# Kernel optimization log

Measured on AMD Instinct MI355X. Metric: run time of the kernel, lower is better.

Reference implementation:

```python
import jax, jax.numpy as jnp
import numpy as np

B, S, D, H = 2, 2048, 2048, 16
HD = D // H


def setup_inputs() -> dict:
    key = jax.random.key(0)
    kx, = jax.random.split(key, 1)
    return {
        "x": jax.random.normal(kx, (B, S, D), dtype=jnp.float32),
        "q_mask": jnp.ones((D, D), dtype=jnp.float32),
        "k_mask": jnp.ones((D, D), dtype=jnp.float32),
        "v_mask": jnp.ones((D, D), dtype=jnp.float32),
        "out_mask": jnp.ones((D, D), dtype=jnp.float32),
        "head_mask": jnp.ones((H,), dtype=jnp.float32),
        "attention_mask": jnp.ones((B, S), dtype=jnp.float32),
        "shared_weight": jnp.float32(1.0),
    }


def reference(x, q_mask, k_mask, v_mask, out_mask, head_mask, attention_mask, shared_weight):
    b, s, d = x.shape
    scale = jnp.float32(HD) ** -0.5

    def shared_linear(inp, mask):
        # F.linear(x, mask * shared_weight): out = inp @ (mask*sw).T
        return jnp.einsum("bsd,ed->bse", inp, mask * shared_weight)

    q = shared_linear(x, q_mask).reshape(b, s, H, HD).transpose(0, 2, 1, 3)  # [B,H,S,HD]
    k = shared_linear(x, k_mask).reshape(b, s, H, HD).transpose(0, 2, 1, 3)
    v = shared_linear(x, v_mask).reshape(b, s, H, HD).transpose(0, 2, 1, 3)

    hm = head_mask.reshape(1, H, 1, 1)
    q, k, v = q * hm, k * hm, v * hm

    scores = jnp.einsum("bhqd,bhkd->bhqk", q, k) * scale  # [B,H,S,S]

    # causal mask: upper triangle (j > i) -> -inf
    causal = jnp.triu(jnp.ones((s, s), dtype=bool), k=1)
    scores = jnp.where(causal, -jnp.inf, scores)

    # additive attention mask: (1 - m) * -10000, broadcast [B,1,1,S]
    scores = scores + (1.0 - attention_mask)[:, None, None, :] * -10000.0

    attn = jax.nn.softmax(scores, axis=-1)  # dropout is identity in eval / p=0

    out = jnp.einsum("bhqk,bhkd->bhqd", attn, v)          # [B,H,S,HD]
    out = out.transpose(0, 2, 1, 3).reshape(b, s, d)       # [B,S,D]
    return shared_linear(out, out_mask)
```

## Files before the change

kernel.cpp:

```cpp
#include <hip/hip_runtime.h>

#define B_  2
#define S_  2048
#define D_  2048
#define H_  16
#define HD_ 128

typedef __bf16 bf16;
typedef __bf16 bf16x4 __attribute__((ext_vector_type(4)));
typedef __bf16 bf16x8 __attribute__((ext_vector_type(8)));
typedef float  f32x4  __attribute__((ext_vector_type(4)));

__device__ __forceinline__ void gld_lds16(const void* g, void* l) {
    __builtin_amdgcn_global_load_lds(
        (const __attribute__((address_space(1))) unsigned int*)g,
        (__attribute__((address_space(3))) unsigned int*)l, 16, 0, 0);
}

__global__ __launch_bounds__(256)
void precast_kernel(const float* __restrict__ x, bf16* __restrict__ xh,
                    bf16* __restrict__ xl) {
    int i = (blockIdx.x * 256 + threadIdx.x) * 8;
    float4 a = *(const float4*)(x + i);
    float4 b = *(const float4*)(x + i + 4);
    float av[8] = {a.x, a.y, a.z, a.w, b.x, b.y, b.z, b.w};
    bf16x8 h8, l8;
#pragma unroll
    for (int e = 0; e < 8; e++) {
        bf16 hv = (bf16)av[e];
        h8[e] = hv;
        l8[e] = (bf16)(av[e] - (float)hv);
    }
    *(bf16x8*)(xh + i) = h8;
    *(bf16x8*)(xl + i) = l8;
}

__global__ __launch_bounds__(256)
void transpose_v(const bf16* __restrict__ vp, bf16* __restrict__ vt) {
    const int bh = blockIdx.x >> 5;
    const int s0 = (blockIdx.x & 31) * 64;
    const int t = threadIdx.x;
    __shared__ bf16 tile[128 * 72];
    const bf16* src = vp + (size_t)bh * S_ * HD_;
    bf16* dst = vt + (size_t)bh * HD_ * S_;
    {
        int r = t >> 2;
        int g = (t & 3) * 4;
#pragma unroll
        for (int w = 0; w < 4; w++) {
            bf16x8 v8 = *(const bf16x8*)&src[(size_t)(s0 + r) * HD_ + (g + w) * 8];
#pragma unroll
            for (int e = 0; e < 8; e++) tile[((g + w) * 8 + e) * 72 + r] = v8[e];
        }
    }
    __syncthreads();
    {
        int d = t >> 1;
        int sg0 = (t & 1) * 4;
#pragma unroll
        for (int w = 0; w < 4; w++) {
            int sg = sg0 + w;
            *(bf16x8*)&dst[(size_t)d * S_ + s0 + sg * 8] =
                *(const bf16x8*)&tile[d * 72 + sg * 8];
        }
    }
}

#define BK 64

template<int MODE>
__global__ __launch_bounds__(256, 3)
void gemm_nt(const bf16* __restrict__ Ah_g, const bf16* __restrict__ Al_g,
             const float* __restrict__ B0, const float* __restrict__ B1,
             const float* __restrict__ B2,
             const float* __restrict__ swp, const float* __restrict__ hm,
             bf16* __restrict__ qh_, bf16* __restrict__ ql_,
             bf16* __restrict__ kh_, bf16* __restrict__ kl_,
             bf16* __restrict__ vp_, float* __restrict__ Cf) {
    const int K = D_;
    __shared__ bf16 Ah[128 * 64];
    __shared__ bf16 Al[128 * 64];
    __shared__ bf16 Bs[128 * 64];
    const int t = threadIdx.x;
    const int wave = t >> 6, lane = t & 63;
    const int wr = wave >> 1, wc = wave & 1;
    const int m0 = blockIdx.y * 128, n0 = blockIdx.x * 128;
    const int lrow = lane & 15, lquad = lane >> 4;
    const float sw = swp[0];

    const int which = (MODE == 0) ? (n0 >> 11) : 0;
    const bool split = (MODE == 0) && (which < 2);

    const float* Bp;
    if (MODE == 0) {
        Bp = (which == 0) ? B0 : ((which == 1) ? B1 : B2);
        Bp += (size_t)(n0 & (D_ - 1)) * K;
    } else {
        Bp = B0 + (size_t)n0 * K;
    }

    const int srow8 = lane >> 3;
    const int sgrp  = lane & 7;
    const int g0 = (lquad)     ^ (lrow & 7);
    const int g1 = (lquad + 4) ^ (lrow & 7);

    f32x4 acc[4][4];
#pragma unroll
    for (int i = 0; i < 4; i++)
#pragma unroll
        for (int j = 0; j < 4; j++) acc[i][j] = (f32x4){0.f, 0.f, 0.f, 0.f};

    for (int k0 = 0; k0 < K; k0 += BK) {
#pragma unroll
        for (int p = 0; p < 4; p++) {
            int r = wave * 32 + p * 8 + srow8;
            int gcol = (sgrp ^ (r & 7)) * 8;
            gld_lds16(Ah_g + (size_t)(m0 + r) * K + k0 + gcol,
                      &Ah[(wave * 32 + p * 8) * 64]);
            if (split)
                gld_lds16(Al_g + (size_t)(m0 + r) * K + k0 + gcol,
                          &Al[(wave * 32 + p * 8) * 64]);
        }
#pragma unroll
        for (int p = 0; p < 4; p++) {
            int r = p * 32 + (t >> 3);
            int gcol = (sgrp ^ (r & 7)) * 8;
            const float* bp = Bp + (size_t)r * K + k0 + gcol;
            float4 blo = *(const float4*)bp;
            float4 bhi = *(const float4*)(bp + 4);
            bf16x8 b8;
            b8[0] = (bf16)(blo.x * sw); b8[1] = (bf16)(blo.y * sw);
            b8[2] = (bf16)(blo.z * sw); b8[3] = (bf16)(blo.w * sw);
            b8[4] = (bf16)(bhi.x * sw); b8[5] = (bf16)(bhi.y * sw);
            b8[6] = (bf16)(bhi.z * sw); b8[7] = (bf16)(bhi.w * sw);
            *(bf16x8*)&Bs[r * 64 + sgrp * 8] = b8;
        }
        __syncthreads();

#pragma unroll
        for (int kk = 0; kk < 2; kk++) {
            const int gA = kk ? g1 : g0;
            bf16x8 afh[4], afl[4], bfr[4];
#pragma unroll
            for (int i = 0; i < 4; i++) {
                int row = wr * 64 + i * 16 + lrow;
                afh[i] = *(const bf16x8*)&Ah[row * 64 + gA * 8];
                if (split) afl[i] = *(const bf16x8*)&Al[row * 64 + gA * 8];
            }
#pragma unroll
            for (int j = 0; j < 4; j++) {
                int row = wc * 64 + j * 16 + lrow;
                bfr[j] = *(const bf16x8*)&Bs[row * 64 + gA * 8];
            }
#pragma unroll
            for (int i = 0; i < 4; i++)
#pragma unroll
                for (int j = 0; j < 4; j++) {
                    acc[i][j] = __builtin_amdgcn_mfma_f32_16x16x32_bf16(
                        afh[i], bfr[j], acc[i][j], 0, 0, 0);
                    if (split)
                        acc[i][j] = __builtin_amdgcn_mfma_f32_16x16x32_bf16(
                            afl[i], bfr[j], acc[i][j], 0, 0, 0);
                }
        }
        __syncthreads();
    }

#pragma unroll
    for (int i = 0; i < 4; i++) {
#pragma unroll
        for (int j = 0; j < 4; j++) {
#pragma unroll
            for (int r = 0; r < 4; r++) {
                int m = m0 + wr * 64 + i * 16 + lquad * 4 + r;
                int n = n0 + wc * 64 + j * 16 + lrow;
                float v = acc[i][j][r];
                if (MODE == 0) {
                    int e = n & (D_ - 1);
                    int h = e >> 7, hd = e & (HD_ - 1);
                    int b = m >> 11, s = m & (S_ - 1);
                    v *= hm[h];
                    size_t idx = (((size_t)b * H_ + h) * S_ + s) * HD_ + hd;
                    if (which == 2) {
                        vp_[idx] = (bf16)v;
                    } else {
                        bf16 hv = (bf16)v;
                        bf16 lv = (bf16)(v - (float)hv);
                        if (which == 0) { qh_[idx] = hv; ql_[idx] = lv; }
                        else            { kh_[idx] = hv; kl_[idx] = lv; }
                    }
                } else {
                    Cf[(size_t)m * D_ + n] = v;
                }
            }
        }
    }
}

__global__ __launch_bounds__(256, 3)
void attn_kernel(const bf16* __restrict__ qh_, const bf16* __restrict__ ql_,
                 const bf16* __restrict__ kh_, const bf16* __restrict__ kl_,
                 const bf16* __restrict__ vt_, const float* __restrict__ am,
                 bf16* __restrict__ outp) {
    const int bh = blockIdx.x & 31;
    const int qblk = 31 - (blockIdx.x >> 5);
    const int b = bh >> 4, h = bh & 15;
    const int i0 = qblk * 64;
    const int t = threadIdx.x, wave = t >> 6, lane = t & 63;
    const int lrow = lane & 15, quad = lane >> 4;

    __shared__ bf16 sh[26624];
    bf16* skh = sh;
    bf16* skl = sh + 8192;
    bf16* svt = sh + 16384;
    bf16* sp  = sh + 24576 + wave * 512;

    const size_t kbase = (size_t)bh * S_ * HD_;
    const size_t vbase = (size_t)bh * HD_ * S_;

    const int qrow = i0 + wave * 16 + lrow;
    bf16x8 qhf[4], qlf[4];
#pragma unroll
    for (int c = 0; c < 4; c++) {
        qhf[c] = *(const bf16x8*)&qh_[kbase + (size_t)qrow * HD_ + c * 32 + quad * 8];
        qlf[c] = *(const bf16x8*)&ql_[kbase + (size_t)qrow * HD_ + c * 32 + quad * 8];
    }

    bf16x8 ones8;
#pragma unroll
    for (int e = 0; e < 8; e++) ones8[e] = (bf16)1.0f;

    float m_i[4];
    f32x4 O[8], Ol;
#pragma unroll
    for (int r = 0; r < 4; r++) m_i[r] = -INFINITY;
#pragma unroll
    for (int n2 = 0; n2 < 8; n2++) O[n2] = (f32x4){0.f, 0.f, 0.f, 0.f};
    Ol = (f32x4){0.f, 0.f, 0.f, 0.f};

    const float scale = 0.08838834764831845f;
    const int iwmin = i0 + wave * 16;
    const int iwmax = iwmin + 15;
    const int nch = (i0 + 64) >> 5;

    {
#pragma unroll
        for (int p = 0; p < 2; p++) {
            int rb = wave * 8 + p * 4;
            int r  = rb + (lane >> 4);
            int gl = ((lane & 15) ^ (r & 7)) * 8;
            gld_lds16(kh_ + kbase + (size_t)r * HD_ + gl, skh + rb * 128);
            gld_lds16(kl_ + kbase + (size_t)r * HD_ + gl, skl + rb * 128);
        }
#pragma unroll
        for (int p = 0; p < 2; p++) {
            int db = wave * 32 + p * 16;
            int d  = db + (lane >> 2);
            int gl = ((lane & 3) ^ (d & 3)) * 8;
            gld_lds16(vt_ + vbase + (size_t)d * S_ + gl, svt + db * 32);
        }
    }

    for (int c = 0; c < nch; c++) {
        __syncthreads();
        if (c + 1 < nch) {
            const int j0s = (c + 1) * 32;
            bf16* dkh = skh + ((c + 1) & 1) * 4096;
            bf16* dkl = skl + ((c + 1) & 1) * 4096;
            bf16* dvt = svt + ((c + 1) & 1) * 4096;
#pragma unroll
            for (int p = 0; p < 2; p++) {
                int rb = wave * 8 + p * 4;
                int r  = rb + (lane >> 4);
                int gl = ((lane & 15) ^ (r & 7)) * 8;
                gld_lds16(kh_ + kbase + (size_t)(j0s + r) * HD_ + gl, dkh + rb * 128);
                gld_lds16(kl_ + kbase + (size_t)(j0s + r) * HD_ + gl, dkl + rb * 128);
            }
#pragma unroll
            for (int p = 0; p < 2; p++) {
                int db = wave * 32 + p * 16;
                int d  = db + (lane >> 2);
                int gl = ((lane & 3) ^ (d & 3)) * 8;
                gld_lds16(vt_ + vbase + (size_t)d * S_ + j0s + gl, dvt + db * 32);
            }
        }

        const int j0 = c * 32;
        if (j0 > iwmax) continue;

        const bf16* kH = skh + (c & 1) * 4096;
        const bf16* kL = skl + (c & 1) * 4096;
        const bf16* vT = svt + (c & 1) * 4096;

        float amadd0 = (1.0f - am[b * S_ + j0 + lrow])      * -10000.0f;
        float amadd1 = (1.0f - am[b * S_ + j0 + 16 + lrow]) * -10000.0f;

        f32x4 s4[2];
        s4[0] = (f32x4){0.f, 0.f, 0.f, 0.f};
        s4[1] = (f32x4){0.f, 0.f, 0.f, 0.f};
#pragma unroll
        for (int cg = 0; cg < 4; cg++) {
#pragma unroll
            for (int nt = 0; nt < 2; nt++) {
                int ka = (nt * 16 + lrow) * 128 + (((cg * 4 + quad) ^ (lrow & 7)) * 8);
                bf16x8 kb8 = *(const bf16x8*)&kH[ka];
                bf16x8 lb8 = *(const bf16x8*)&kL[ka];
                s4[nt] = __builtin_amdgcn_mfma_f32_16x16x32_bf16(qhf[cg], kb8, s4[nt], 0, 0, 0);
                s4[nt] = __builtin_amdgcn_mfma_f32_16x16x32_bf16(qhf[cg], lb8, s4[nt], 0, 0, 0);
                s4[nt] = __builtin_amdgcn_mfma_f32_16x16x32_bf16(qlf[cg], kb8, s4[nt], 0, 0, 0);
            }
        }

        const bool msk = (j0 + 31 > iwmin);
#pragma unroll
        for (int r = 0; r < 4; r++) {
            const int irow = iwmin + quad * 4 + r;
            float x0 = s4[0][r] * scale + amadd0;
            float x1 = s4[1][r] * scale + amadd1;
            if (msk) {
                if (j0 + lrow > irow)      x0 = -INFINITY;
                if (j0 + 16 + lrow > irow) x1 = -INFINITY;
            }
            float mx = fmaxf(x0, x1);
#pragma unroll
            for (int off = 1; off < 16; off <<= 1) mx = fmaxf(mx, __shfl_xor(mx, off));
            float mnew = fmaxf(m_i[r], mx);
            float alpha = __expf(m_i[r] - mnew);
            m_i[r] = mnew;
            float p0 = __expf(x0 - mnew);
            float p1 = __expf(x1 - mnew);
            Ol[r] *= alpha;
#pragma unroll
            for (int n2 = 0; n2 < 8; n2++) O[n2][r] *= alpha;
            const int rl = quad * 4 + r;
            sp[rl * 32 + (((lrow >> 3) ^ (rl & 3)) * 8) + (lrow & 7)] = (bf16)p0;
            sp[rl * 32 + ((((lrow >> 3) + 2) ^ (rl & 3)) * 8) + (lrow & 7)] = (bf16)p1;
        }
        __asm__ volatile("s_waitcnt lgkmcnt(0)" ::: "memory");

        bf16x8 pf = *(const bf16x8*)&sp[lrow * 32 + ((quad ^ (lrow & 3)) * 8)];
#pragma unroll
        for (int n2 = 0; n2 < 8; n2++) {
            bf16x8 vf8 = *(const bf16x8*)&vT[(n2 * 16 + lrow) * 32 + ((quad ^ (lrow & 3)) * 8)];
            O[n2] = __builtin_amdgcn_mfma_f32_16x16x32_bf16(pf, vf8, O[n2], 0, 0, 0);
        }
        Ol = __builtin_amdgcn_mfma_f32_16x16x32_bf16(pf, ones8, Ol, 0, 0, 0);
    }

    float inv[4];
#pragma unroll
    for (int r = 0; r < 4; r++) inv[r] = 1.0f / Ol[r];
#pragma unroll
    for (int n2 = 0; n2 < 8; n2++)
#pragma unroll
        for (int r = 0; r < 4; r++) {
            int srow = i0 + wave * 16 + quad * 4 + r;
            outp[((size_t)(b * S_ + srow)) * D_ + h * HD_ + n2 * 16 + lrow] =
                (bf16)(O[n2][r] * inv[r]);
        }
}

extern "C" void kernel_launch(void* const* d_in, const int* in_sizes, int n_in,
                              void* d_out, int out_size, void* d_ws, size_t ws_size,
                              hipStream_t stream) {
    const float* x  = (const float*)d_in[0];
    const float* qm = (const float*)d_in[1];
    const float* km = (const float*)d_in[2];
    const float* vm = (const float*)d_in[3];
    const float* om = (const float*)d_in[4];
    const float* hm = (const float*)d_in[5];
    const float* am = (const float*)d_in[6];
    const float* sw = (const float*)d_in[7];
    float* out = (float*)d_out;

    const size_t P = (size_t)B_ * H_ * S_ * HD_ * sizeof(bf16);
    char* ws = (char*)d_ws;
    bf16* xh = (bf16*)(ws + 0 * P);
    bf16* xl = (bf16*)(ws + 1 * P);
    bf16* qh = (bf16*)(ws + 2 * P);
    bf16* ql = (bf16*)(ws + 3 * P);
    bf16* kh = (bf16*)(ws + 4 * P);
    bf16* kl = (bf16*)(ws + 5 * P);
    bf16* vp = (bf16*)d_out;
    bf16* vt = (bf16*)((char*)d_out + P);
    bf16* attn_out = (bf16*)(ws + 0 * P);

    precast_kernel<<<(B_ * S_ * D_) / (256 * 8), 256, 0, stream>>>(x, xh, xl);

    gemm_nt<0><<<dim3(48, 32), 256, 0, stream>>>(
        xh, xl, qm, km, vm, sw, hm, qh, ql, kh, kl, vp, nullptr);

    transpose_v<<<1024, 256, 0, stream>>>(vp, vt);

    attn_kernel<<<1024, 256, 0, stream>>>(qh, ql, kh, kl, vt, am, attn_out);

    gemm_nt<1><<<dim3(16, 32), 256, 0, stream>>>(
        attn_out, nullptr, om, nullptr, nullptr, sw, hm,
        nullptr, nullptr, nullptr, nullptr, nullptr, out);
}
```

Before: 496.7 us.

## Single-buffer attention K/V tiles and raise occupancy to five blocks

Drops the double-buffered K/V prefetch in the attention kernel and uses single LDS buffers loaded synchronously each chunk, with two barriers per iteration. This roughly halves LDS use so the launch bound can rise from 3 to 5 blocks per CU, relying on more resident waves to hide global latency instead of software prefetch. It also folds log2(e) into the scale and mask constant so the softmax can use exp2f. The cost is that load latency is no longer overlapped within a block, plus an extra barrier per chunk and tighter register limits.

```diff
diff --git a/kernel.cpp b/kernel.cpp
--- a/kernel.cpp
+++ b/kernel.cpp
@@ -197,7 +197,7 @@
     }
 }
 
-__global__ __launch_bounds__(256, 3)
+__global__ __launch_bounds__(256, 5)
 void attn_kernel(const bf16* __restrict__ qh_, const bf16* __restrict__ ql_,
                  const bf16* __restrict__ kh_, const bf16* __restrict__ kl_,
                  const bf16* __restrict__ vt_, const float* __restrict__ am,
@@ -209,11 +209,10 @@
     const int t = threadIdx.x, wave = t >> 6, lane = t & 63;
     const int lrow = lane & 15, quad = lane >> 4;
 
-    __shared__ bf16 sh[26624];
-    bf16* skh = sh;
-    bf16* skl = sh + 8192;
-    bf16* svt = sh + 16384;
-    bf16* sp  = sh + 24576 + wave * 512;
+    __shared__ bf16 skh[32 * 128];
+    __shared__ bf16 skl[32 * 128];
+    __shared__ bf16 svt[128 * 32];
+    __shared__ bf16 spm[4][16 * 32];
 
     const size_t kbase = (size_t)bh * S_ * HD_;
     const size_t vbase = (size_t)bh * HD_ * S_;
@@ -238,113 +237,86 @@
     for (int n2 = 0; n2 < 8; n2++) O[n2] = (f32x4){0.f, 0.f, 0.f, 0.f};
     Ol = (f32x4){0.f, 0.f, 0.f, 0.f};
 
-    const float scale = 0.08838834764831845f;
+    const float scale2 = 0.08838834764831845f * 1.44269504088896f;
     const int iwmin = i0 + wave * 16;
     const int iwmax = iwmin + 15;
     const int nch = (i0 + 64) >> 5;
 
-    {
+    for (int c = 0; c < nch; c++) {
+        const int j0 = c * 32;
+        __syncthreads();
 #pragma unroll
         for (int p = 0; p < 2; p++) {
             int rb = wave * 8 + p * 4;
             int r  = rb + (lane >> 4);
             int gl = ((lane & 15) ^ (r & 7)) * 8;
-            gld_lds16(kh_ + kbase + (size_t)r * HD_ + gl, skh + rb * 128);
-            gld_lds16(kl_ + kbase + (size_t)r * HD_ + gl, skl + rb * 128);
+            gld_lds16(kh_ + kbase + (size_t)(j0 + r) * HD_ + gl, &skh[rb * 128]);
+            gld_lds16(kl_ + kbase + (size_t)(j0 + r) * HD_ + gl, &skl[rb * 128]);
         }
 #pragma unroll
         for (int p = 0; p < 2; p++) {
             int db = wave * 32 + p * 16;
             int d  = db + (lane >> 2);
             int gl = ((lane & 3) ^ (d & 3)) * 8;
-            gld_lds16(vt_ + vbase + (size_t)d * S_ + gl, svt + db * 32);
-        }
-    }
-
-    for (int c = 0; c < nch; c++) {
+            gld_lds16(vt_ + vbase + (size_t)d * S_ + j0 + gl, &svt[db * 32]);
+        }
         __syncthreads();
-        if (c + 1 < nch) {
-            const int j0s = (c + 1) * 32;
-            bf16* dkh = skh + ((c + 1) & 1) * 4096;
-            bf16* dkl = skl + ((c + 1) & 1) * 4096;
-            bf16* dvt = svt + ((c + 1) & 1) * 4096;
-#pragma unroll
-            for (int p = 0; p < 2; p++) {
-                int rb = wave * 8 + p * 4;
-                int r  = rb + (lane >> 4);
-                int gl = ((lane & 15) ^ (r & 7)) * 8;
-                gld_lds16(kh_ + kbase + (size_t)(j0s + r) * HD_ + gl, dkh + rb * 128);
-                gld_lds16(kl_ + kbase + (size_t)(j0s + r) * HD_ + gl, dkl + rb * 128);
-            }
-#pragma unroll
-            for (int p = 0; p < 2; p++) {
-                int db = wave * 32 + p * 16;
-                int d  = db + (lane >> 2);
-                int gl = ((lane & 3) ^ (d & 3)) * 8;
-                gld_lds16(vt_ + vbase + (size_t)d * S_ + j0s + gl, dvt + db * 32);
-            }
-        }
-
-        const int j0 = c * 32;
-        if (j0 > iwmax) continue;
-
-        const bf16* kH = skh + (c & 1) * 4096;
-        const bf16* kL = skl + (c & 1) * 4096;
-        const bf16* vT = svt + (c & 1) * 4096;
-
-        float amadd0 = (1.0f - am[b * S_ + j0 + lrow])      * -10000.0f;
-        float amadd1 = (1.0f - am[b * S_ + j0 + 16 + lrow]) * -10000.0f;
-
-        f32x4 s4[2];
-        s4[0] = (f32x4){0.f, 0.f, 0.f, 0.f};
-        s4[1] = (f32x4){0.f, 0.f, 0.f, 0.f};
-#pragma unroll
-        for (int cg = 0; cg < 4; cg++) {
-#pragma unroll
-            for (int nt = 0; nt < 2; nt++) {
-                int ka = (nt * 16 + lrow) * 128 + (((cg * 4 + quad) ^ (lrow & 7)) * 8);
-                bf16x8 kb8 = *(const bf16x8*)&kH[ka];
-                bf16x8 lb8 = *(const bf16x8*)&kL[ka];
-                s4[nt] = __builtin_amdgcn_mfma_f32_16x16x32_bf16(qhf[cg], kb8, s4[nt], 0, 0, 0);
-                s4[nt] = __builtin_amdgcn_mfma_f32_16x16x32_bf16(qhf[cg], lb8, s4[nt], 0, 0, 0);
-                s4[nt] = __builtin_amdgcn_mfma_f32_16x16x32_bf16(qlf[cg], kb8, s4[nt], 0, 0, 0);
-            }
-        }
-
-        const bool msk = (j0 + 31 > iwmin);
-#pragma unroll
-        for (int r = 0; r < 4; r++) {
-            const int irow = iwmin + quad * 4 + r;
-            float x0 = s4[0][r] * scale + amadd0;
-            float x1 = s4[1][r] * scale + amadd1;
-            if (msk) {
-                if (j0 + lrow > irow)      x0 = -INFINITY;
-                if (j0 + 16 + lrow > irow) x1 = -INFINITY;
-            }
-            float mx = fmaxf(x0, x1);
-#pragma unroll
-            for (int off = 1; off < 16; off <<= 1) mx = fmaxf(mx, __shfl_xor(mx, off));
-            float mnew = fmaxf(m_i[r], mx);
-            float alpha = __expf(m_i[r] - mnew);
-            m_i[r] = mnew;
-            float p0 = __expf(x0 - mnew);
-            float p1 = __expf(x1 - mnew);
-            Ol[r] *= alpha;
-#pragma unroll
-            for (int n2 = 0; n2 < 8; n2++) O[n2][r] *= alpha;
-            const int rl = quad * 4 + r;
-            sp[rl * 32 + (((lrow >> 3) ^ (rl & 3)) * 8) + (lrow & 7)] = (bf16)p0;
-            sp[rl * 32 + ((((lrow >> 3) + 2) ^ (rl & 3)) * 8) + (lrow & 7)] = (bf16)p1;
-        }
-        __asm__ volatile("s_waitcnt lgkmcnt(0)" ::: "memory");
-
-        bf16x8 pf = *(const bf16x8*)&sp[lrow * 32 + ((quad ^ (lrow & 3)) * 8)];
-#pragma unroll
-        for (int n2 = 0; n2 < 8; n2++) {
-            bf16x8 vf8 = *(const bf16x8*)&vT[(n2 * 16 + lrow) * 32 + ((quad ^ (lrow & 3)) * 8)];
-            O[n2] = __builtin_amdgcn_mfma_f32_16x16x32_bf16(pf, vf8, O[n2], 0, 0, 0);
-        }
-        Ol = __builtin_amdgcn_mfma_f32_16x16x32_bf16(pf, ones8, Ol, 0, 0, 0);
+
+        if (j0 <= iwmax) {
+            float amadd0 = (1.0f - am[b * S_ + j0 + lrow])      * -14426.950408f;
+            float amadd1 = (1.0f - am[b * S_ + j0 + 16 + lrow]) * -14426.950408f;
+
+            f32x4 s4[2];
+            s4[0] = (f32x4){0.f, 0.f, 0.f, 0.f};
+            s4[1] = (f32x4){0.f, 0.f, 0.f, 0.f};
+#pragma unroll
+            for (int cg = 0; cg < 4; cg++) {
+#pragma unroll
+                for (int nt = 0; nt < 2; nt++) {
+                    int ka = (nt * 16 + lrow) * 128 + (((cg * 4 + quad) ^ (lrow & 7)) * 8);
+                    bf16x8 kb8 = *(const bf16x8*)&skh[ka];
+                    bf16x8 lb8 = *(const bf16x8*)&skl[ka];
+                    s4[nt] = __builtin_amdgcn_mfma_f32_16x16x32_bf16(qhf[cg], kb8, s4[nt], 0, 0, 0);
+                    s4[nt] = __builtin_amdgcn_mfma_f32_16x16x32_bf16(qhf[cg], lb8, s4[nt], 0, 0, 0);
+                    s4[nt] = __builtin_amdgcn_mfma_f32_16x16x32_bf16(qlf[cg], kb8, s4[nt], 0, 0, 0);
+                }
+            }
+
+            const bool msk = (j0 + 31 > iwmin);
+#pragma unroll
+            for (int r = 0; r < 4; r++) {
+                const int irow = iwmin + quad * 4 + r;
+                float x0 = s4[0][r] * scale2 + amadd0;
+                float x1 = s4[1][r] * scale2 + amadd1;
+                if (msk) {
+                    if (j0 + lrow > irow)      x0 = -INFINITY;
+                    if (j0 + 16 + lrow > irow) x1 = -INFINITY;
+                }
+                float mx = fmaxf(x0, x1);
+#pragma unroll
+                for (int off = 1; off < 16; off <<= 1) mx = fmaxf(mx, __shfl_xor(mx, off));
+                float mnew = fmaxf(m_i[r], mx);
+                float alpha = exp2f(m_i[r] - mnew);
+                m_i[r] = mnew;
+                float p0 = exp2f(x0 - mnew);
+                float p1 = exp2f(x1 - mnew);
+                Ol[r] *= alpha;
+#pragma unroll
+                for (int n2 = 0; n2 < 8; n2++) O[n2][r] *= alpha;
+                const int rl = quad * 4 + r;
+                spm[wave][rl * 32 + (((lrow >> 3) ^ (rl & 3)) * 8) + (lrow & 7)] = (bf16)p0;
+                spm[wave][rl * 32 + ((((lrow >> 3) + 2) ^ (rl & 3)) * 8) + (lrow & 7)] = (bf16)p1;
+            }
+            __asm__ volatile("s_waitcnt lgkmcnt(0)" ::: "memory");
+
+            bf16x8 pf = *(const bf16x8*)&spm[wave][lrow * 32 + ((quad ^ (lrow & 3)) * 8)];
+#pragma unroll
+            for (int n2 = 0; n2 < 8; n2++) {
+                bf16x8 vf8 = *(const bf16x8*)&svt[(n2 * 16 + lrow) * 32 + ((quad ^ (lrow & 3)) * 8)];
+                O[n2] = __builtin_amdgcn_mfma_f32_16x16x32_bf16(pf, vf8, O[n2], 0, 0, 0);
+            }
+            Ol = __builtin_amdgcn_mfma_f32_16x16x32_bf16(pf, ones8, Ol, 0, 0, 0);
+        }
     }
 
     float inv[4];
```

New measurement: 704.5 us. 1.42x slower.
